# Kernel optimization log

Measured on AMD Instinct MI355X. Metric: run time of the kernel, lower is better.

## Reference

```python
import jax, jax.numpy as jnp
import numpy as np


def _gcn_norm(edge_index, num_nodes):
    """Add self-loops and compute symmetric normalization coeffs (PyG GCNConv default)."""
    loop = jnp.arange(num_nodes, dtype=edge_index.dtype)
    row = jnp.concatenate([edge_index[0], loop])  # source nodes
    col = jnp.concatenate([edge_index[1], loop])  # target nodes
    deg = jax.ops.segment_sum(jnp.ones_like(col, dtype=jnp.float32), col,
                              num_segments=num_nodes)
    dinv = jnp.where(deg > 0, jax.lax.rsqrt(deg), 0.0)
    norm = dinv[row] * dinv[col]  # [E + N]
    return row, col, norm


def _gcn_conv(x, W, b, row, col, norm, num_nodes):
    xw = x @ W                                   # [N, out]
    msg = xw[row] * norm[:, None]                # gather + scale, [E+N, out]
    out = jax.ops.segment_sum(msg, col, num_segments=num_nodes)  # scatter-add
    return out + b


def setup_inputs() -> dict:
    key = jax.random.key(0)
    ks = jax.random.split(key, 12)
    N, E, F, H, C, G = 100000, 1600000, 64, 64, 10, 128
    x = jax.random.normal(ks[0], (N, F), dtype=jnp.float32)
    edge_index = jax.random.randint(ks[1], (2, E), 0, N, dtype=jnp.int64)
    batch = jnp.sort(jax.random.randint(ks[2], (N,), 0, G, dtype=jnp.int64))
    def glorot(k, fan_in, fan_out):
        s = jnp.sqrt(6.0 / (fan_in + fan_out))
        return jax.random.uniform(k, (fan_in, fan_out), jnp.float32, -s, s)
    return {
        "x": x, "edge_index": edge_index, "batch": batch, "num_graphs": G,
        "W0": glorot(ks[3], F, H), "b0": jnp.zeros((H,), jnp.float32),
        "W1": glorot(ks[4], H, H), "b1": jnp.zeros((H,), jnp.float32),
        "W2": glorot(ks[5], H, H), "b2": jnp.zeros((H,), jnp.float32),
        "Wro": glorot(ks[6], H, C), "bro": jnp.zeros((C,), jnp.float32),
    }


def reference(x, edge_index, batch, num_graphs, W0, b0, W1, b1, W2, b2, Wro, bro):
    N = x.shape[0]
    row, col, norm = _gcn_norm(edge_index, N)
    for W, b in ((W0, b0), (W1, b1), (W2, b2)):
        x = jax.nn.silu(_gcn_conv(x, W, b, row, col, norm, N))
        # dropout p=0.0 / eval mode -> identity
    # global_mean_pool over batch ids
    sums = jax.ops.segment_sum(x, batch, num_segments=num_graphs)   # [G, H]
    cnts = jax.ops.segment_sum(jnp.ones((N,), x.dtype), batch, num_segments=num_graphs)
    pooled = sums / jnp.maximum(cnts, 1.0)[:, None]
    # readout: Linear + ReLU (make_mlp with hidden_layers=1), then log_softmax
    logits = jax.nn.relu(pooled @ Wro + bro)
    return jax.nn.log_softmax(logits, axis=1)
```

## Files before the change

kernel.cpp:

```cpp
#include <hip/hip_runtime.h>
#include <hip/hip_fp16.h>


#define CH 128
#define BSH 7
#define BNODES 128

typedef _Float16 half8 __attribute__((ext_vector_type(8)));
typedef float float4v __attribute__((ext_vector_type(4)));

__global__ __launch_bounds__(256) void k_hist(const int* __restrict__ col, int E, int Ec, int NB,
                                              int* __restrict__ histG) {
    __shared__ int h[1024];
    int c = blockIdx.x, tid = threadIdx.x;
    for (int i = tid; i < NB; i += 256) h[i] = 0;
    __syncthreads();
    int lo = c * Ec, hi = min(E, lo + Ec);
    for (int e = lo + tid; e < hi; e += 256) atomicAdd(&h[col[e] >> BSH], 1);
    __syncthreads();
    for (int i = tid; i < NB; i += 256) histG[c * NB + i] = h[i];
}

__global__ void k_scanb(int* __restrict__ histG, int NB, int* __restrict__ btot) {
    int b = blockIdx.x;
    int l = threadIdx.x;
    int v0 = histG[l * NB + b];
    int v1 = histG[(64 + l) * NB + b];
    int p0 = v0, p1 = v1;
    for (int off = 1; off < 64; off <<= 1) {
        int t0 = __shfl_up(p0, off);
        int t1 = __shfl_up(p1, off);
        if (l >= off) { p0 += t0; p1 += t1; }
    }
    int A = __shfl(p0, 63);
    int T = A + __shfl(p1, 63);
    histG[l * NB + b] = p0 - v0;
    histG[(64 + l) * NB + b] = A + p1 - v1;
    if (l == 0) btot[b] = T;
}

__global__ void k_scant(const int* __restrict__ btot, int NB, int E, int* __restrict__ bstart) {
    __shared__ int s[1024];
    int tid = threadIdx.x;
    int v = (tid < NB) ? btot[tid] : 0;
    s[tid] = v;
    __syncthreads();
    for (int off = 1; off < 1024; off <<= 1) {
        int t = (tid >= off) ? s[tid - off] : 0;
        __syncthreads();
        s[tid] += t;
        __syncthreads();
    }
    if (tid < NB) bstart[tid] = s[tid] - v;
    if (tid == 0) bstart[NB] = E;
}

__global__ __launch_bounds__(256) void k_scatter(const int* __restrict__ col, const int* __restrict__ row,
                                                 int E, int Ec, int NB,
                                                 const int* __restrict__ histG,
                                                 const int* __restrict__ bstart,
                                                 unsigned int* __restrict__ edges) {
    __shared__ int cur[1024];
    int c = blockIdx.x, tid = threadIdx.x;
    for (int i = tid; i < NB; i += 256) cur[i] = bstart[i] + histG[c * NB + i];
    __syncthreads();
    int lo = c * Ec, hi = min(E, lo + Ec);
    for (int e = lo + tid; e < hi; e += 256) {
        int cc = col[e];
        int b = cc >> BSH;
        int pos = atomicAdd(&cur[b], 1);
        edges[pos] = (unsigned int)row[e] | ((unsigned int)(cc & (BNODES - 1)) << 25);
    }
}

__global__ __launch_bounds__(256) void k_sort2(const unsigned int* __restrict__ edges,
                                               const int* __restrict__ bstart, int N, int E, int NB,
                                               int* __restrict__ srcs, int* __restrict__ starts,
                                               float* __restrict__ dinv) {
    __shared__ int cnt[BNODES];
    __shared__ int cur[BNODES];
    int b = blockIdx.x, tid = threadIdx.x;
    if (tid < BNODES) cnt[tid] = 0;
    __syncthreads();
    int lo = bstart[b], hi = bstart[b + 1];
    for (int e = lo + tid; e < hi; e += 256) atomicAdd(&cnt[edges[e] >> 25], 1);
    __syncthreads();
    if (tid < 64) {
        int v0 = cnt[tid], v1 = cnt[64 + tid];
        int p0 = v0, p1 = v1;
        for (int off = 1; off < 64; off <<= 1) {
            int t0 = __shfl_up(p0, off);
            int t1 = __shfl_up(p1, off);
            if (tid >= off) { p0 += t0; p1 += t1; }
        }
        int A = __shfl(p0, 63);
        cur[tid] = lo + p0 - v0;
        cur[64 + tid] = lo + A + p1 - v1;
    }
    __syncthreads();
    int ng = b * BNODES + tid;
    if (tid < BNODES && ng < N) {
        starts[ng] = cur[tid];
        dinv[ng] = rsqrtf((float)cnt[tid] + 1.0f);
    }
    if (b == 0 && tid == 0) starts[N] = E;
    __syncthreads();
    for (int e = lo + tid; e < hi; e += 256) {
        unsigned int p = edges[e];
        int pos = atomicAdd(&cur[p >> 25], 1);
        srcs[pos] = (int)((p & 0x1FFFFFFu) << 3);
    }
}

template <int IN_HALF>
__global__ __launch_bounds__(256) void k_gemm(const void* __restrict__ xin,
                                              const float* __restrict__ W,
                                              const float* __restrict__ dinv,
                                              __half* __restrict__ yh, int N) {
    __shared__ float sW[64 * 64];
    int tid = threadIdx.x;
    for (int k = tid; k < 4096; k += 256) sW[k] = W[k];
    __syncthreads();
    int lane = tid & 63, wv = tid >> 6;
    int c16 = lane & 15, kg = lane >> 4;
    half8 bf[4][2];
#pragma unroll
    for (int ct = 0; ct < 4; ++ct)
#pragma unroll
        for (int ks = 0; ks < 2; ++ks)
#pragma unroll
            for (int j = 0; j < 8; ++j)
                bf[ct][ks][j] = (_Float16)sW[(ks * 32 + kg * 8 + j) * 64 + ct * 16 + c16];

    int tiles = (N + 15) >> 4;
    for (int t = blockIdx.x * 4 + wv; t < tiles; t += gridDim.x * 4) {
        int base = t << 4;
        int arow = base + c16;
        half8 af0, af1;
        if (arow < N) {
            if (IN_HALF) {
                const __half* xh = (const __half*)xin;
                af0 = *(const half8*)(xh + (size_t)arow * 64 + kg * 8);
                af1 = *(const half8*)(xh + (size_t)arow * 64 + 32 + kg * 8);
            } else {
                const float* xf = (const float*)xin;
                float4 u0 = *(const float4*)(xf + (size_t)arow * 64 + kg * 8);
                float4 u1 = *(const float4*)(xf + (size_t)arow * 64 + kg * 8 + 4);
                float4 u2 = *(const float4*)(xf + (size_t)arow * 64 + 32 + kg * 8);
                float4 u3 = *(const float4*)(xf + (size_t)arow * 64 + 32 + kg * 8 + 4);
                af0[0]=(_Float16)u0.x; af0[1]=(_Float16)u0.y; af0[2]=(_Float16)u0.z; af0[3]=(_Float16)u0.w;
                af0[4]=(_Float16)u1.x; af0[5]=(_Float16)u1.y; af0[6]=(_Float16)u1.z; af0[7]=(_Float16)u1.w;
                af1[0]=(_Float16)u2.x; af1[1]=(_Float16)u2.y; af1[2]=(_Float16)u2.z; af1[3]=(_Float16)u2.w;
                af1[4]=(_Float16)u3.x; af1[5]=(_Float16)u3.y; af1[6]=(_Float16)u3.z; af1[7]=(_Float16)u3.w;
            }
        } else {
#pragma unroll
            for (int j = 0; j < 8; ++j) { af0[j] = (_Float16)0.f; af1[j] = (_Float16)0.f; }
        }
#pragma unroll
        for (int ct = 0; ct < 4; ++ct) {
            float4v c = {0.f, 0.f, 0.f, 0.f};
            c = __builtin_amdgcn_mfma_f32_16x16x32_f16(af0, bf[ct][0], c, 0, 0, 0);
            c = __builtin_amdgcn_mfma_f32_16x16x32_f16(af1, bf[ct][1], c, 0, 0, 0);
#pragma unroll
            for (int q = 0; q < 4; ++q) {
                int rr = base + kg * 4 + q;
                if (rr < N) yh[(size_t)rr * 64 + ct * 16 + c16] = __float2half_rn(c[q] * dinv[rr]);
            }
        }
    }
}

__global__ __launch_bounds__(256) void k_agg(const int* __restrict__ starts,
                                             const int* __restrict__ srcs,
                                             const __half* __restrict__ yh,
                                             const float* __restrict__ dinv,
                                             const float* __restrict__ b,
                                             __half* __restrict__ xh, int N) {
    int wv = (blockIdx.x * blockDim.x + threadIdx.x) >> 6;
    int lane = threadIdx.x & 63;
    int g = lane >> 3, i = lane & 7;
    int node = wv * 8 + g;
    bool valid = node < N;
    const float4* y4 = (const float4*)yh;
    __half2 a0, a1, a2, a3;
    a0 = a1 = a2 = a3 = __half2half2(__ushort_as_half((unsigned short)0));
    int s = 0, t = 0;
    if (valid) {
        s = starts[node]; t = starts[node + 1];
        float4 raw = y4[(size_t)node * 8 + i];
        const __half2* h = (const __half2*)&raw;
        a0 = h[0]; a1 = h[1]; a2 = h[2]; a3 = h[3];
    }
    int e = s;
    for (; e + 1 < t; e += 2) {
        int s0 = srcs[e], s1 = srcs[e + 1];
        float4 r0 = y4[(size_t)s0 + i];
        float4 r1 = y4[(size_t)s1 + i];
        const __half2* h0 = (const __half2*)&r0;
        const __half2* h1 = (const __half2*)&r1;
        a0 = __hadd2(__hadd2(a0, h0[0]), h1[0]);
        a1 = __hadd2(__hadd2(a1, h0[1]), h1[1]);
        a2 = __hadd2(__hadd2(a2, h0[2]), h1[2]);
        a3 = __hadd2(__hadd2(a3, h0[3]), h1[3]);
    }
    if (e < t) {
        int s0 = srcs[e];
        float4 r0 = y4[(size_t)s0 + i];
        const __half2* h0 = (const __half2*)&r0;
        a0 = __hadd2(a0, h0[0]); a1 = __hadd2(a1, h0[1]);
        a2 = __hadd2(a2, h0[2]); a3 = __hadd2(a3, h0[3]);
    }
    if (valid) {
        float d = dinv[node];
        float4 b0 = ((const float4*)b)[2 * i];
        float4 b1 = ((const float4*)b)[2 * i + 1];
        float bb[8] = {b0.x, b0.y, b0.z, b0.w, b1.x, b1.y, b1.z, b1.w};
        float2 f0 = __half22float2(a0), f1 = __half22float2(a1);
        float2 f2 = __half22float2(a2), f3 = __half22float2(a3);
        float sums[8] = {f0.x, f0.y, f1.x, f1.y, f2.x, f2.y, f3.x, f3.y};
        float o[8];
#pragma unroll
        for (int f = 0; f < 8; ++f) {
            float v = d * sums[f] + bb[f];
            o[f] = v / (1.f + __expf(-v));
        }
        float4 outv;
        __half2* oh = (__half2*)&outv;
#pragma unroll
        for (int p = 0; p < 4; ++p) oh[p] = __float22half2_rn(make_float2(o[2 * p], o[2 * p + 1]));
        ((float4*)xh)[(size_t)node * 8 + i] = outv;
    }
}

__global__ void k_pool_readout(const __half2* __restrict__ xh2, const int* __restrict__ batch, int N,
                               const float* __restrict__ Wro, const float* __restrict__ bro,
                               float* __restrict__ out, int C) {
    int g = blockIdx.x;
    int tid = threadIdx.x, wave = tid >> 6, lane = tid & 63;
    int grp = lane >> 5, i = lane & 31;
    __shared__ float part[4][64];
    __shared__ float pooled[64];
    __shared__ float logits[32];
    int lo = 0, hb = N;
    while (lo < hb) { int m = (lo + hb) >> 1; if (batch[m] < g) lo = m + 1; else hb = m; }
    int lo2 = lo, hi2 = N;
    while (lo2 < hi2) { int m = (lo2 + hi2) >> 1; if (batch[m] < g + 1) lo2 = m + 1; else hi2 = m; }
    int hi = lo2;
    float ax = 0.f, ay = 0.f;
    for (int r = lo + wave * 2 + grp; r < hi; r += 8) {
        float2 v = __half22float2(xh2[(size_t)r * 32 + i]);
        ax += v.x; ay += v.y;
    }
    ax += __shfl_xor(ax, 32);
    ay += __shfl_xor(ay, 32);
    if (grp == 0) { part[wave][2 * i] = ax; part[wave][2 * i + 1] = ay; }
    __syncthreads();
    if (tid < 64) {
        float cntf = fmaxf((float)(hi - lo), 1.0f);
        pooled[tid] = (part[0][tid] + part[1][tid] + part[2][tid] + part[3][tid]) / cntf;
    }
    __syncthreads();
    if (tid < C) {
        float a = bro[tid];
        for (int k = 0; k < 64; ++k) a += pooled[k] * Wro[k * C + tid];
        logits[tid] = fmaxf(a, 0.f);
    }
    __syncthreads();
    if (tid == 0) {
        float m = -1e30f;
        for (int c = 0; c < C; ++c) m = fmaxf(m, logits[c]);
        float sum = 0.f;
        for (int c = 0; c < C; ++c) sum += __expf(logits[c] - m);
        float lse = m + __logf(sum);
        for (int c = 0; c < C; ++c) out[g * C + c] = logits[c] - lse;
    }
}

static inline size_t align256(size_t v) { return (v + 255) & ~(size_t)255; }

extern "C" void kernel_launch(void* const* d_in, const int* in_sizes, int n_in,
                              void* d_out, int out_size, void* d_ws, size_t ws_size,
                              hipStream_t stream) {
    const float* x    = (const float*)d_in[0];
    const int*   ei   = (const int*)d_in[1];
    const int*   batch= (const int*)d_in[2];
    const float* W[3] = {(const float*)d_in[4], (const float*)d_in[6], (const float*)d_in[8]};
    const float* b[3] = {(const float*)d_in[5], (const float*)d_in[7], (const float*)d_in[9]};
    const float* Wro  = (const float*)d_in[10];
    const float* bro  = (const float*)d_in[11];

    int N = in_sizes[2];
    int E = in_sizes[1] / 2;
    int C = in_sizes[10] / 64;
    int G = out_size / C;

    const int* row = ei;
    const int* col = ei + E;

    int NB = (N + BNODES - 1) >> BSH;
    int Ec = (E + CH - 1) / CH;

    char* ws = (char*)d_ws;
    size_t off = 0;
    float* dinv    = (float*)(ws + off);        off = align256(off + (size_t)N * 4);
    int*   histG   = (int*)(ws + off);          off = align256(off + (size_t)CH * NB * 4);
    int*   btot    = (int*)(ws + off);          off = align256(off + (size_t)NB * 4);
    int*   bstart  = (int*)(ws + off);          off = align256(off + (size_t)(NB + 1) * 4);
    unsigned int* edges = (unsigned int*)(ws + off); off = align256(off + (size_t)E * 4);
    int*   srcs    = (int*)(ws + off);          off = align256(off + (size_t)E * 4);
    int*   starts  = (int*)(ws + off);          off = align256(off + (size_t)(N + 1) * 4);
    __half* yh     = (__half*)(ws + off);       off = align256(off + (size_t)N * 64 * 2);
    __half* xh     = (__half*)(ws + off);       off = align256(off + (size_t)N * 64 * 2);

    k_hist<<<CH, 256, 0, stream>>>(col, E, Ec, NB, histG);
    k_scanb<<<NB, 64, 0, stream>>>(histG, NB, btot);
    k_scant<<<1, 1024, 0, stream>>>(btot, NB, E, bstart);
    k_scatter<<<CH, 256, 0, stream>>>(col, row, E, Ec, NB, histG, bstart, edges);
    k_sort2<<<NB, 256, 0, stream>>>(edges, bstart, N, E, NB, srcs, starts, dinv);

    int aggB = (N + 31) / 32;
    int gemmB = 1568;

    k_gemm<0><<<gemmB, 256, 0, stream>>>(x, W[0], dinv, yh, N);
    k_agg<<<aggB, 256, 0, stream>>>(starts, srcs, yh, dinv, b[0], xh, N);
    k_gemm<1><<<gemmB, 256, 0, stream>>>(xh, W[1], dinv, yh, N);
    k_agg<<<aggB, 256, 0, stream>>>(starts, srcs, yh, dinv, b[1], xh, N);
    k_gemm<1><<<gemmB, 256, 0, stream>>>(xh, W[2], dinv, yh, N);
    k_agg<<<aggB, 256, 0, stream>>>(starts, srcs, yh, dinv, b[2], xh, N);

    k_pool_readout<<<G, 256, 0, stream>>>((const __half2*)xh, batch, N, Wro, bro, (float*)d_out, C);
}
```

Before: 249.8 us.

## Widen CSR build parallelism and unroll aggregation gather by four

Doubles the number of histogram/scatter chunks and generalizes the per-bucket scan to four 64-lane segments. It launches the scatter with 1024 threads and the per-bucket sort with 512 threads, and unrolls the aggregation edge loop to issue four gathers at a time. The aim is more parallelism and memory-level parallelism in the preprocessing and gather phases, at the cost of more LDS atomic contention per block and higher register pressure in the aggregation kernel.

Measured after the change: 226.4 us. 9.3% less time.

```diff
diff --git a/kernel.cpp b/kernel.cpp
--- a/kernel.cpp
+++ b/kernel.cpp
@@ -2,7 +2,7 @@
 #include <hip/hip_fp16.h>
 
 
-#define CH 128
+#define CH 256
 #define BSH 7
 #define BNODES 128
 
@@ -24,19 +24,24 @@
 __global__ void k_scanb(int* __restrict__ histG, int NB, int* __restrict__ btot) {
     int b = blockIdx.x;
     int l = threadIdx.x;
-    int v0 = histG[l * NB + b];
-    int v1 = histG[(64 + l) * NB + b];
-    int p0 = v0, p1 = v1;
+    int v[4], p[4];
+#pragma unroll
+    for (int k = 0; k < 4; ++k) { v[k] = histG[(k * 64 + l) * NB + b]; p[k] = v[k]; }
     for (int off = 1; off < 64; off <<= 1) {
-        int t0 = __shfl_up(p0, off);
-        int t1 = __shfl_up(p1, off);
-        if (l >= off) { p0 += t0; p1 += t1; }
-    }
-    int A = __shfl(p0, 63);
-    int T = A + __shfl(p1, 63);
-    histG[l * NB + b] = p0 - v0;
-    histG[(64 + l) * NB + b] = A + p1 - v1;
-    if (l == 0) btot[b] = T;
+#pragma unroll
+        for (int k = 0; k < 4; ++k) {
+            int t = __shfl_up(p[k], off);
+            if (l >= off) p[k] += t;
+        }
+    }
+    int acc = 0;
+#pragma unroll
+    for (int k = 0; k < 4; ++k) {
+        int tot = __shfl(p[k], 63);
+        histG[(k * 64 + l) * NB + b] = acc + p[k] - v[k];
+        acc += tot;
+    }
+    if (l == 0) btot[b] = acc;
 }
 
 __global__ void k_scant(const int* __restrict__ btot, int NB, int E, int* __restrict__ bstart) {
@@ -55,17 +60,17 @@
     if (tid == 0) bstart[NB] = E;
 }
 
-__global__ __launch_bounds__(256) void k_scatter(const int* __restrict__ col, const int* __restrict__ row,
-                                                 int E, int Ec, int NB,
-                                                 const int* __restrict__ histG,
-                                                 const int* __restrict__ bstart,
-                                                 unsigned int* __restrict__ edges) {
+__global__ __launch_bounds__(1024) void k_scatter(const int* __restrict__ col, const int* __restrict__ row,
+                                                  int E, int Ec, int NB,
+                                                  const int* __restrict__ histG,
+                                                  const int* __restrict__ bstart,
+                                                  unsigned int* __restrict__ edges) {
     __shared__ int cur[1024];
     int c = blockIdx.x, tid = threadIdx.x;
-    for (int i = tid; i < NB; i += 256) cur[i] = bstart[i] + histG[c * NB + i];
+    for (int i = tid; i < NB; i += 1024) cur[i] = bstart[i] + histG[c * NB + i];
     __syncthreads();
     int lo = c * Ec, hi = min(E, lo + Ec);
-    for (int e = lo + tid; e < hi; e += 256) {
+    for (int e = lo + tid; e < hi; e += 1024) {
         int cc = col[e];
         int b = cc >> BSH;
         int pos = atomicAdd(&cur[b], 1);
@@ -73,7 +78,7 @@
     }
 }
 
-__global__ __launch_bounds__(256) void k_sort2(const unsigned int* __restrict__ edges,
+__global__ __launch_bounds__(512) void k_sort2(const unsigned int* __restrict__ edges,
                                                const int* __restrict__ bstart, int N, int E, int NB,
                                                int* __restrict__ srcs, int* __restrict__ starts,
                                                float* __restrict__ dinv) {
@@ -83,7 +88,7 @@
     if (tid < BNODES) cnt[tid] = 0;
     __syncthreads();
     int lo = bstart[b], hi = bstart[b + 1];
-    for (int e = lo + tid; e < hi; e += 256) atomicAdd(&cnt[edges[e] >> 25], 1);
+    for (int e = lo + tid; e < hi; e += 512) atomicAdd(&cnt[edges[e] >> 25], 1);
     __syncthreads();
     if (tid < 64) {
         int v0 = cnt[tid], v1 = cnt[64 + tid];
@@ -105,7 +110,7 @@
     }
     if (b == 0 && tid == 0) starts[N] = E;
     __syncthreads();
-    for (int e = lo + tid; e < hi; e += 256) {
+    for (int e = lo + tid; e < hi; e += 512) {
         unsigned int p = edges[e];
         int pos = atomicAdd(&cur[p >> 25], 1);
         srcs[pos] = (int)((p & 0x1FFFFFFu) << 3);
@@ -193,18 +198,22 @@
         a0 = h[0]; a1 = h[1]; a2 = h[2]; a3 = h[3];
     }
     int e = s;
-    for (; e + 1 < t; e += 2) {
-        int s0 = srcs[e], s1 = srcs[e + 1];
+    for (; e + 3 < t; e += 4) {
+        int s0 = srcs[e], s1 = srcs[e + 1], s2 = srcs[e + 2], s3 = srcs[e + 3];
         float4 r0 = y4[(size_t)s0 + i];
         float4 r1 = y4[(size_t)s1 + i];
+        float4 r2 = y4[(size_t)s2 + i];
+        float4 r3 = y4[(size_t)s3 + i];
         const __half2* h0 = (const __half2*)&r0;
         const __half2* h1 = (const __half2*)&r1;
-        a0 = __hadd2(__hadd2(a0, h0[0]), h1[0]);
-        a1 = __hadd2(__hadd2(a1, h0[1]), h1[1]);
-        a2 = __hadd2(__hadd2(a2, h0[2]), h1[2]);
-        a3 = __hadd2(__hadd2(a3, h0[3]), h1[3]);
-    }
-    if (e < t) {
+        const __half2* h2 = (const __half2*)&r2;
+        const __half2* h3 = (const __half2*)&r3;
+        a0 = __hadd2(__hadd2(__hadd2(a0, h0[0]), h1[0]), __hadd2(h2[0], h3[0]));
+        a1 = __hadd2(__hadd2(__hadd2(a1, h0[1]), h1[1]), __hadd2(h2[1], h3[1]));
+        a2 = __hadd2(__hadd2(__hadd2(a2, h0[2]), h1[2]), __hadd2(h2[2], h3[2]));
+        a3 = __hadd2(__hadd2(__hadd2(a3, h0[3]), h1[3]), __hadd2(h2[3], h3[3]));
+    }
+    for (; e < t; ++e) {
         int s0 = srcs[e];
         float4 r0 = y4[(size_t)s0 + i];
         const __half2* h0 = (const __half2*)&r0;
@@ -316,8 +325,8 @@
     k_hist<<<CH, 256, 0, stream>>>(col, E, Ec, NB, histG);
     k_scanb<<<NB, 64, 0, stream>>>(histG, NB, btot);
     k_scant<<<1, 1024, 0, stream>>>(btot, NB, E, bstart);
-    k_scatter<<<CH, 256, 0, stream>>>(col, row, E, Ec, NB, histG, bstart, edges);
-    k_sort2<<<NB, 256, 0, stream>>>(edges, bstart, N, E, NB, srcs, starts, dinv);
+    k_scatter<<<CH, 1024, 0, stream>>>(col, row, E, Ec, NB, histG, bstart, edges);
+    k_sort2<<<NB, 512, 0, stream>>>(edges, bstart, N, E, NB, srcs, starts, dinv);
 
     int aggB = (N + 31) / 32;
     int gemmB = 1568;
```
